# Performance work log

Measured on AMD Instinct MI355X. Metric: run time of the kernel, lower is better.

Reference implementation:

```python
import jax, jax.numpy as jnp
import numpy as np

N = 50000
E = 800000
IN_CH = 128
HID = 64
HEADS = 4
NEG_SLOPE_GAT = 0.2   # PyG GATConv default negative_slope
NEG_SLOPE_ACT = 0.01  # nn.LeakyReLU default
LN_EPS = 1e-5


def segment_softmax(logits, seg, num):
    # softmax over edges grouped by destination node (PyG softmax semantics)
    m = jax.ops.segment_max(logits, seg, num_segments=num)
    m = jnp.where(jnp.isfinite(m), m, 0.0)
    e = jnp.exp(logits - m[seg])
    s = jax.ops.segment_sum(e, seg, num_segments=num)
    return e / (s[seg] + 1e-16)


def gat_conv(x, edge_index, W, a_src, a_dst, b, heads, out_ch):
    n = x.shape[0]
    loop = jnp.arange(n)
    src = jnp.concatenate([edge_index[0], loop])  # message sources (x_j)
    dst = jnp.concatenate([edge_index[1], loop])  # aggregation targets (x_i)
    h = (x @ W).reshape(n, heads, out_ch)          # [N,H,C]
    alpha_src = (h * a_src).sum(-1)                # [N,H]
    alpha_dst = (h * a_dst).sum(-1)                # [N,H]
    alpha = alpha_src[src] + alpha_dst[dst]        # [E',H]
    alpha = jax.nn.leaky_relu(alpha, NEG_SLOPE_GAT)
    alpha = segment_softmax(alpha, dst, n)
    msg = h[src] * alpha[:, :, None]               # [E',H,C] gathered messages
    out = jax.ops.segment_sum(msg, dst, num_segments=n)  # [N,H,C]
    return out.reshape(n, heads * out_ch) + b


def layer_norm(x, gamma, beta):
    mu = x.mean(-1, keepdims=True)
    var = ((x - mu) ** 2).mean(-1, keepdims=True)
    return (x - mu) * jax.lax.rsqrt(var + LN_EPS) * gamma + beta


def setup_inputs() -> dict:
    key = jax.random.key(0)
    ks = jax.random.split(key, 12)
    d1 = HEADS * HID
    inp = {
        "x": jax.random.normal(ks[0], (N, IN_CH), dtype=jnp.float32),
        "edge_index": jax.random.randint(ks[1], (2, E), 0, N, dtype=jnp.int64),
        "W1": jax.random.normal(ks[2], (IN_CH, d1), dtype=jnp.float32) * 0.05,
        "a_src1": jax.random.normal(ks[3], (HEADS, HID), dtype=jnp.float32) * 0.1,
        "a_dst1": jax.random.normal(ks[4], (HEADS, HID), dtype=jnp.float32) * 0.1,
        "b1": jnp.zeros((d1,), dtype=jnp.float32),
        "gamma": jnp.ones((d1,), dtype=jnp.float32),
        "beta": jnp.zeros((d1,), dtype=jnp.float32),
        "W2": jax.random.normal(ks[5], (d1, HID), dtype=jnp.float32) * 0.05,
        "a_src2": jax.random.normal(ks[6], (1, HID), dtype=jnp.float32) * 0.1,
        "a_dst2": jax.random.normal(ks[7], (1, HID), dtype=jnp.float32) * 0.1,
        "b2": jnp.zeros((HID,), dtype=jnp.float32),
    }
    return inp


def reference(x, edge_index, W1, a_src1, a_dst1, b1, gamma, beta, W2, a_src2, a_dst2, b2):
    h = gat_conv(x, edge_index, W1, a_src1, a_dst1, b1, HEADS, HID)  # [N, H*HID]
    h = layer_norm(h, gamma, beta)
    h = jax.nn.leaky_relu(h, NEG_SLOPE_ACT)
    out = gat_conv(h, edge_index, W2, a_src2, a_dst2, b2, 1, HID)    # [N, HID]
    return out
```

## Files before the change

### kernel.cpp

```cpp
#include <hip/hip_runtime.h>
#include <hip/hip_bf16.h>

#define IN_CH 128
#define D1 256
#define HID 64
#define HEADS 4
#define CAP 48

typedef _Float16 h16;
typedef __attribute__((ext_vector_type(4))) _Float16 half4v;
typedef __attribute__((ext_vector_type(8))) _Float16 half8v;
typedef __attribute__((ext_vector_type(4))) float f32x4;

__device__ __forceinline__ float lrelu02(float v) { return v > 0.f ? v : 0.2f * v; }
__device__ __forceinline__ float lrelu001(float v) { return v > 0.f ? v : 0.01f * v; }
__device__ __forceinline__ unsigned short h2b(h16 h) {
    union { h16 h; unsigned short b; } c; c.h = h; return c.b;
}
__device__ __forceinline__ h16 b2h(unsigned short b) {
    union { unsigned short b; h16 h; } c; c.b = b; return c.h;
}

__global__ __launch_bounds__(256) void prep_kernel(const float* __restrict__ W1,
                                                   const float* __restrict__ W2,
                                                   const float* __restrict__ a_src1,
                                                   const float* __restrict__ a_dst1,
                                                   const float* __restrict__ a_src2,
                                                   const float* __restrict__ a_dst2,
                                                   h16* __restrict__ w1t,
                                                   h16* __restrict__ w2t) {
    const int b = blockIdx.x;
    const int t = threadIdx.x;
    if (b == 0) {
        for (int k = 0; k < IN_CH; ++k) w1t[t * IN_CH + k] = (h16)W1[k * D1 + t];
    } else if (b == 1) {
        if (t < HID)
            for (int k = 0; k < D1; ++k) w2t[t * D1 + k] = (h16)W2[k * HID + t];
        for (int i = t; i < 14 * D1; i += 256) w2t[66 * D1 + i] = (h16)0.f;
    } else if (b == 2) {
        for (int o = t; o < 1024; o += 256) {
            int v = o >> 7, k = o & 127;
            int h = v & 3;
            const float* avec = (v >> 2) ? (a_dst1 + h * HID) : (a_src1 + h * HID);
            const float* wrow = W1 + k * D1 + h * HID;
            float s = 0.f;
            for (int c = 0; c < HID; ++c) s += wrow[c] * avec[c];
            w1t[(256 + v) * IN_CH + k] = (h16)s;
            w1t[(264 + v) * IN_CH + k] = (h16)0.f;
        }
    } else {
        for (int o = t; o < 512; o += 256) {
            int v = o >> 8, k = o & 255;
            const float* avec = v ? a_dst2 : a_src2;
            const float* wrow = W2 + k * HID;
            float s = 0.f;
            for (int c = 0; c < HID; ++c) s += wrow[c] * avec[c];
            w2t[(64 + v) * D1 + k] = (h16)s;
        }
    }
}

__global__ __launch_bounds__(256) void gemm1_mfma(const float* __restrict__ x,
                                                  const h16* __restrict__ w1t,
                                                  h16* __restrict__ h1,
                                                  float* __restrict__ asad, int n) {
    const int wave = threadIdx.x >> 6, lane = threadIdx.x & 63;
    const int r = lane & 15, ksel = lane >> 4;
    const int rowBase = blockIdx.x * 64 + wave * 16;
    const int row_a = rowBase + r;
    half8v a[4];
    if (row_a < n) {
        const float* xrow = x + (size_t)row_a * IN_CH + ksel * 8;
        #pragma unroll
        for (int kk = 0; kk < 4; ++kk) {
            float4 u = *(const float4*)(xrow + kk * 32);
            float4 v = *(const float4*)(xrow + kk * 32 + 4);
            half8v av;
            av[0] = (h16)u.x; av[1] = (h16)u.y; av[2] = (h16)u.z; av[3] = (h16)u.w;
            av[4] = (h16)v.x; av[5] = (h16)v.y; av[6] = (h16)v.z; av[7] = (h16)v.w;
            a[kk] = av;
        }
    } else {
        #pragma unroll
        for (int kk = 0; kk < 4; ++kk) a[kk] = (half8v){};
    }
    f32x4 acc[17];
    #pragma unroll
    for (int ct = 0; ct < 17; ++ct) acc[ct] = (f32x4){0.f, 0.f, 0.f, 0.f};
    #pragma unroll
    for (int ct = 0; ct < 17; ++ct) {
        const h16* wrow = w1t + (size_t)(ct * 16 + r) * IN_CH + ksel * 8;
        #pragma unroll
        for (int kk = 0; kk < 4; ++kk) {
            half8v b = *(const half8v*)(wrow + kk * 32);
            acc[ct] = __builtin_amdgcn_mfma_f32_16x16x32_f16(a[kk], b, acc[ct], 0, 0, 0);
        }
    }
    #pragma unroll
    for (int i = 0; i < 4; ++i) {
        int row = rowBase + ksel * 4 + i;
        if (row < n) {
            #pragma unroll
            for (int ct = 0; ct < 16; ++ct)
                h1[(size_t)row * D1 + ct * 16 + r] = (h16)acc[ct][i];
            if (r < 8) asad[(size_t)row * 8 + r] = acc[16][i];
        }
    }
}

__global__ __launch_bounds__(256) void scatter_ewt_kernel(const int* __restrict__ ei,
                                                          int* __restrict__ cnt,
                                                          const float* __restrict__ asad,
                                                          int4* __restrict__ esd, int nE) {
    int e = blockIdx.x * 256 + threadIdx.x;
    if (e >= nE) return;
    int src = ei[e];
    int dst = ei[nE + e];
    int pos = atomicAdd(&cnt[dst], 1);
    if (pos >= CAP) return;
    float4 as = *(const float4*)&asad[(size_t)src * 8];
    float4 ad = *(const float4*)&asad[(size_t)dst * 8 + 4];
    unsigned short b0 = h2b((h16)expf(lrelu02(as.x + ad.x)));
    unsigned short b1 = h2b((h16)expf(lrelu02(as.y + ad.y)));
    unsigned short b2 = h2b((h16)expf(lrelu02(as.z + ad.z)));
    unsigned short b3 = h2b((h16)expf(lrelu02(as.w + ad.w)));
    int w01 = (int)b0 | ((int)b1 << 16);
    int w23 = (int)b2 | ((int)b3 << 16);
    esd[(size_t)dst * CAP + pos] = make_int4(src, w01, w23, 0);
}

__global__ __launch_bounds__(256) void gemm2_mfma(const h16* __restrict__ hm,
                                                  const h16* __restrict__ w2t,
                                                  h16* __restrict__ h2,
                                                  float* __restrict__ asad2, int n) {
    const int wave = threadIdx.x >> 6, lane = threadIdx.x & 63;
    const int r = lane & 15, ksel = lane >> 4;
    const int rowBase = blockIdx.x * 64 + wave * 16;
    const h16* xrow = hm + (size_t)(rowBase + r) * D1 + ksel * 8;
    half8v a[8];
    #pragma unroll
    for (int kk = 0; kk < 8; ++kk) a[kk] = *(const half8v*)(xrow + kk * 32);
    f32x4 acc[5];
    #pragma unroll
    for (int ct = 0; ct < 5; ++ct) acc[ct] = (f32x4){0.f, 0.f, 0.f, 0.f};
    #pragma unroll
    for (int ct = 0; ct < 5; ++ct) {
        const h16* wrow = w2t + (size_t)(ct * 16 + r) * D1 + ksel * 8;
        #pragma unroll
        for (int kk = 0; kk < 8; ++kk) {
            half8v b = *(const half8v*)(wrow + kk * 32);
            acc[ct] = __builtin_amdgcn_mfma_f32_16x16x32_f16(a[kk], b, acc[ct], 0, 0, 0);
        }
    }
    #pragma unroll
    for (int i = 0; i < 4; ++i) {
        int row = rowBase + ksel * 4 + i;
        if (row < n) {
            #pragma unroll
            for (int ct = 0; ct < 4; ++ct)
                h2[(size_t)row * HID + ct * 16 + r] = (h16)acc[ct][i];
            if (r < 2) asad2[(size_t)row * 2 + r] = acc[4][i];
        }
    }
}

__global__ __launch_bounds__(256) void gather1_kernel(const h16* __restrict__ h1,
                                                      const float* __restrict__ asad,
                                                      const int4* __restrict__ esd,
                                                      const int* __restrict__ cnt,
                                                      const float* __restrict__ b1,
                                                      const float* __restrict__ gamma,
                                                      const float* __restrict__ beta,
                                                      h16* __restrict__ hmid,
                                                      int n, int npad) {
    const int lane = threadIdx.x & 63;
    const int node = (blockIdx.x * 256 + threadIdx.x) >> 6;
    if (node >= npad) return;
    if (node >= n) {
        half4v z = {};
        *(half4v*)&hmid[(size_t)node * D1 + lane * 4] = z;
        return;
    }
    const int hh = lane >> 4;
    const int hsel = hh & 1;
    const unsigned* ep  = (const unsigned*)esd;
    const unsigned* epw = ep + 1 + (hh >> 1);
    const float wself = expf(lrelu02(asad[(size_t)node * 8 + hh] +
                                     asad[(size_t)node * 8 + 4 + hh]));
    half4v sv = *(const half4v*)&h1[(size_t)node * D1 + lane * 4];
    h16 wsh = (h16)wself;
    half4v acc = sv * (half4v){wsh, wsh, wsh, wsh};
    float den = wself;
    int d = cnt[node]; d = d < CAP ? d : CAP;
    const int beg = node * CAP;
    const int end = beg + ((d + 7) & ~7);
    int j = beg;
    for (; j + 8 <= end; j += 8) {
        int s0 = (int)ep[(size_t)(j + 0) * 4];
        int s1 = (int)ep[(size_t)(j + 1) * 4];
        int s2 = (int)ep[(size_t)(j + 2) * 4];
        int s3 = (int)ep[(size_t)(j + 3) * 4];
        int s4 = (int)ep[(size_t)(j + 4) * 4];
        int s5 = (int)ep[(size_t)(j + 5) * 4];
        int s6 = (int)ep[(size_t)(j + 6) * 4];
        int s7 = (int)ep[(size_t)(j + 7) * 4];
        unsigned u0 = epw[(size_t)(j + 0) * 4];
        unsigned u1 = epw[(size_t)(j + 1) * 4];
        unsigned u2 = epw[(size_t)(j + 2) * 4];
        unsigned u3 = epw[(size_t)(j + 3) * 4];
        unsigned u4 = epw[(size_t)(j + 4) * 4];
        unsigned u5 = epw[(size_t)(j + 5) * 4];
        unsigned u6 = epw[(size_t)(j + 6) * 4];
        unsigned u7 = epw[(size_t)(j + 7) * 4];
        half4v r0 = *(const half4v*)&h1[(size_t)s0 * D1 + lane * 4];
        half4v r1 = *(const half4v*)&h1[(size_t)s1 * D1 + lane * 4];
        half4v r2 = *(const half4v*)&h1[(size_t)s2 * D1 + lane * 4];
        half4v r3 = *(const half4v*)&h1[(size_t)s3 * D1 + lane * 4];
        half4v r4 = *(const half4v*)&h1[(size_t)s4 * D1 + lane * 4];
        half4v r5 = *(const half4v*)&h1[(size_t)s5 * D1 + lane * 4];
        half4v r6 = *(const half4v*)&h1[(size_t)s6 * D1 + lane * 4];
        half4v r7 = *(const half4v*)&h1[(size_t)s7 * D1 + lane * 4];
        h16 w0 = b2h((unsigned short)(hsel ? u0 >> 16 : u0 & 0xffff));
        h16 w1 = b2h((unsigned short)(hsel ? u1 >> 16 : u1 & 0xffff));
        h16 w2 = b2h((unsigned short)(hsel ? u2 >> 16 : u2 & 0xffff));
        h16 w3 = b2h((unsigned short)(hsel ? u3 >> 16 : u3 & 0xffff));
        h16 w4 = b2h((unsigned short)(hsel ? u4 >> 16 : u4 & 0xffff));
        h16 w5 = b2h((unsigned short)(hsel ? u5 >> 16 : u5 & 0xffff));
        h16 w6 = b2h((unsigned short)(hsel ? u6 >> 16 : u6 & 0xffff));
        h16 w7 = b2h((unsigned short)(hsel ? u7 >> 16 : u7 & 0xffff));
        acc += r0 * (half4v){w0, w0, w0, w0};
        acc += r1 * (half4v){w1, w1, w1, w1};
        acc += r2 * (half4v){w2, w2, w2, w2};
        acc += r3 * (half4v){w3, w3, w3, w3};
        acc += r4 * (half4v){w4, w4, w4, w4};
        acc += r5 * (half4v){w5, w5, w5, w5};
        acc += r6 * (half4v){w6, w6, w6, w6};
        acc += r7 * (half4v){w7, w7, w7, w7};
        den += (float)w0 + (float)w1 + (float)w2 + (float)w3
             + (float)w4 + (float)w5 + (float)w6 + (float)w7;
    }
    float4 accf = make_float4((float)acc[0], (float)acc[1], (float)acc[2], (float)acc[3]);
    float inv = 1.f / (den + 1e-16f);
    float4 bv = *(const float4*)&b1[lane * 4];
    float4 y;
    y.x = accf.x * inv + bv.x; y.y = accf.y * inv + bv.y;
    y.z = accf.z * inv + bv.z; y.w = accf.w * inv + bv.w;
    float s = y.x + y.y + y.z + y.w;
    #pragma unroll
    for (int off = 1; off < 64; off <<= 1) s += __shfl_xor(s, off, 64);
    float mu = s * (1.f / 256.f);
    float4 dx;
    dx.x = y.x - mu; dx.y = y.y - mu; dx.z = y.z - mu; dx.w = y.w - mu;
    float sq = dx.x * dx.x + dx.y * dx.y + dx.z * dx.z + dx.w * dx.w;
    #pragma unroll
    for (int off = 1; off < 64; off <<= 1) sq += __shfl_xor(sq, off, 64);
    float rs = rsqrtf(sq * (1.f / 256.f) + 1e-5f);
    float4 g = *(const float4*)&gamma[lane * 4];
    float4 be = *(const float4*)&beta[lane * 4];
    half4v o;
    o.x = (h16)lrelu001(dx.x * rs * g.x + be.x);
    o.y = (h16)lrelu001(dx.y * rs * g.y + be.y);
    o.z = (h16)lrelu001(dx.z * rs * g.z + be.z);
    o.w = (h16)lrelu001(dx.w * rs * g.w + be.w);
    *(half4v*)&hmid[(size_t)node * D1 + lane * 4] = o;
}

__global__ __launch_bounds__(256) void gather2_kernel(const h16* __restrict__ h2,
                                                      const float* __restrict__ asad2,
                                                      const int4* __restrict__ esd,
                                                      const int* __restrict__ cnt,
                                                      const float* __restrict__ b2,
                                                      float* __restrict__ out, int n) {
    const int lane = threadIdx.x & 63;
    const int node = (blockIdx.x * 256 + threadIdx.x) >> 6;
    if (node >= n) return;
    const int li = lane & 15, eh = lane >> 4;
    const int c0 = li * 4;
    const float ad_n = asad2[(size_t)node * 2 + 1];
    float acc[4] = {0.f, 0.f, 0.f, 0.f};
    float den = 0.f;
    if (eh == 0) {
        float w0 = expf(lrelu02(asad2[(size_t)node * 2] + ad_n));
        half4v sv = *(const half4v*)&h2[(size_t)node * HID + c0];
        #pragma unroll
        for (int i = 0; i < 4; ++i) acc[i] = (float)sv[i] * w0;
        den = w0;
    }
    int d = cnt[node]; d = d < CAP ? d : CAP;
    const int beg = node * CAP;
    const int end = beg + d;
    int j = beg;
    for (; j + 8 <= end; j += 8) {
        int s0 = esd[j + eh].x;
        int s1 = esd[j + 4 + eh].x;
        float a0 = asad2[(size_t)s0 * 2], a1 = asad2[(size_t)s1 * 2];
        half4v r0 = *(const half4v*)&h2[(size_t)s0 * HID + c0];
        half4v r1 = *(const half4v*)&h2[(size_t)s1 * HID + c0];
        float w0 = expf(lrelu02(a0 + ad_n));
        float w1 = expf(lrelu02(a1 + ad_n));
        #pragma unroll
        for (int i = 0; i < 4; ++i) {
            acc[i] = fmaf((float)r0[i], w0, acc[i]);
            acc[i] = fmaf((float)r1[i], w1, acc[i]);
        }
        den += w0 + w1;
    }
    for (; j < end; j += 4) {
        int e = j + eh;
        bool v = e < end;
        int s = v ? esd[e].x : 0;
        float w = v ? expf(lrelu02(asad2[(size_t)s * 2] + ad_n)) : 0.f;
        half4v r = *(const half4v*)&h2[(size_t)s * HID + c0];
        #pragma unroll
        for (int i = 0; i < 4; ++i) acc[i] = fmaf((float)r[i], w, acc[i]);
        den += w;
    }
    #pragma unroll
    for (int i = 0; i < 4; ++i) {
        acc[i] += __shfl_xor(acc[i], 32, 64);
        acc[i] += __shfl_xor(acc[i], 16, 64);
    }
    den += __shfl_xor(den, 32, 64);
    den += __shfl_xor(den, 16, 64);
    if (lane < 16) {
        float inv = 1.f / (den + 1e-16f);
        float4 bv = *(const float4*)&b2[c0];
        float4 o;
        o.x = acc[0] * inv + bv.x;
        o.y = acc[1] * inv + bv.y;
        o.z = acc[2] * inv + bv.z;
        o.w = acc[3] * inv + bv.w;
        *(float4*)&out[(size_t)node * HID + c0] = o;
    }
}

extern "C" void kernel_launch(void* const* d_in, const int* in_sizes, int n_in,
                              void* d_out, int out_size, void* d_ws, size_t ws_size,
                              hipStream_t stream) {
    const float* x      = (const float*)d_in[0];
    const int*   ei     = (const int*)d_in[1];
    const float* W1     = (const float*)d_in[2];
    const float* a_src1 = (const float*)d_in[3];
    const float* a_dst1 = (const float*)d_in[4];
    const float* b1     = (const float*)d_in[5];
    const float* gamma  = (const float*)d_in[6];
    const float* beta   = (const float*)d_in[7];
    const float* W2     = (const float*)d_in[8];
    const float* a_src2 = (const float*)d_in[9];
    const float* a_dst2 = (const float*)d_in[10];
    const float* b2     = (const float*)d_in[11];
    float* out = (float*)d_out;

    const int N = in_sizes[0] / IN_CH;
    const int E = in_sizes[1] / 2;
    const int NP = (N + 63) & ~63;

    float* ws = (float*)d_ws;
    size_t off = 0;
    h16*   h1   = (h16*)(ws + off); off += (size_t)128 * N;
    h16*   hmid = (h16*)(ws + off); off += (size_t)128 * NP;
    h16*   h2   = (h16*)(ws + off); off += (size_t)32 * N;
    float* asad = ws + off;         off += (size_t)8 * N;
    float* asad2= ws + off;         off += (size_t)2 * N;
    h16* w1t = (h16*)(ws + off); off += 17408;
    h16* w2t = (h16*)(ws + off); off += 10240;
    off = (off + 3) & ~(size_t)3;
    int* cnt = (int*)(ws + off); off += N;
    off = (off + 3) & ~(size_t)3;
    int4* esd = (int4*)(ws + off); off += (size_t)4 * ((size_t)N * CAP + 8);
    const size_t memsetBytes = (size_t)(ws + off) - (size_t)cnt;

    const int nodeBlocks  = (N + 3) / 4;
    const int nodeBlocksP = (NP + 3) / 4;
    const int nThreadBlocksE = (E + 255) / 256;

    hipMemsetAsync(cnt, 0, memsetBytes, stream);
    prep_kernel<<<4, 256, 0, stream>>>(W1, W2, a_src1, a_dst1, a_src2, a_dst2, w1t, w2t);
    gemm1_mfma<<<NP / 64, 256, 0, stream>>>(x, w1t, h1, asad, N);
    scatter_ewt_kernel<<<nThreadBlocksE, 256, 0, stream>>>(ei, cnt, asad, esd, E);
    gather1_kernel<<<nodeBlocksP, 256, 0, stream>>>(h1, asad, esd, cnt,
                                                    b1, gamma, beta, hmid, N, NP);
    gemm2_mfma<<<NP / 64, 256, 0, stream>>>(hmid, w2t, h2, asad2, N);
    gather2_kernel<<<nodeBlocks, 256, 0, stream>>>(h2, asad2, esd, cnt, b2, out, N);
}
```

Before: 226.9 us.

## Split attention-logit GEMM out and co-schedule main GEMM with edge scatter

The first GEMM is split in two. A small kernel computes only the per-node attention logits (asad), and the main 256-column projection is fused into the edge-scatter kernel as extra blocks. The scatter depends only on asad, so the compute-bound GEMM blocks and the atomic-heavy, memory-bound scatter blocks can run concurrently in one launch. In exchange, x is read twice, and one launch has to carry both the register-heavy MFMA path and the light scatter path, which may reduce occupancy for the scatter blocks.

```diff
diff --git a/kernel.cpp b/kernel.cpp
--- a/kernel.cpp
+++ b/kernel.cpp
@@ -60,10 +60,9 @@
     }
 }
 
-__global__ __launch_bounds__(256) void gemm1_mfma(const float* __restrict__ x,
-                                                  const h16* __restrict__ w1t,
-                                                  h16* __restrict__ h1,
-                                                  float* __restrict__ asad, int n) {
+__global__ __launch_bounds__(256) void asadg_kernel(const float* __restrict__ x,
+                                                    const h16* __restrict__ w1t,
+                                                    float* __restrict__ asad, int n) {
     const int wave = threadIdx.x >> 6, lane = threadIdx.x & 63;
     const int r = lane & 15, ksel = lane >> 4;
     const int rowBase = blockIdx.x * 64 + wave * 16;
@@ -84,11 +83,69 @@
         #pragma unroll
         for (int kk = 0; kk < 4; ++kk) a[kk] = (half8v){};
     }
-    f32x4 acc[17];
-    #pragma unroll
-    for (int ct = 0; ct < 17; ++ct) acc[ct] = (f32x4){0.f, 0.f, 0.f, 0.f};
-    #pragma unroll
-    for (int ct = 0; ct < 17; ++ct) {
+    f32x4 acc = (f32x4){0.f, 0.f, 0.f, 0.f};
+    const h16* wrow = w1t + (size_t)(256 + r) * IN_CH + ksel * 8;
+    #pragma unroll
+    for (int kk = 0; kk < 4; ++kk) {
+        half8v b = *(const half8v*)(wrow + kk * 32);
+        acc = __builtin_amdgcn_mfma_f32_16x16x32_f16(a[kk], b, acc, 0, 0, 0);
+    }
+    #pragma unroll
+    for (int i = 0; i < 4; ++i) {
+        int row = rowBase + ksel * 4 + i;
+        if (row < n && r < 8) asad[(size_t)row * 8 + r] = acc[i];
+    }
+}
+
+__global__ __launch_bounds__(256) void scatter_gemm1_kernel(
+        const int* __restrict__ ei, int* __restrict__ cnt,
+        const float* __restrict__ asad, int4* __restrict__ esd, int nE, int nbE,
+        const float* __restrict__ x, const h16* __restrict__ w1t,
+        h16* __restrict__ h1, int n) {
+    if (blockIdx.x < (unsigned)nbE) {
+        int e = blockIdx.x * 256 + threadIdx.x;
+        if (e >= nE) return;
+        int src = ei[e];
+        int dst = ei[nE + e];
+        int pos = atomicAdd(&cnt[dst], 1);
+        if (pos >= CAP) return;
+        float4 as = *(const float4*)&asad[(size_t)src * 8];
+        float4 ad = *(const float4*)&asad[(size_t)dst * 8 + 4];
+        unsigned short b0 = h2b((h16)expf(lrelu02(as.x + ad.x)));
+        unsigned short b1 = h2b((h16)expf(lrelu02(as.y + ad.y)));
+        unsigned short b2 = h2b((h16)expf(lrelu02(as.z + ad.z)));
+        unsigned short b3 = h2b((h16)expf(lrelu02(as.w + ad.w)));
+        int w01 = (int)b0 | ((int)b1 << 16);
+        int w23 = (int)b2 | ((int)b3 << 16);
+        esd[(size_t)dst * CAP + pos] = make_int4(src, w01, w23, 0);
+        return;
+    }
+    const int bid = blockIdx.x - nbE;
+    const int wave = threadIdx.x >> 6, lane = threadIdx.x & 63;
+    const int r = lane & 15, ksel = lane >> 4;
+    const int rowBase = bid * 64 + wave * 16;
+    const int row_a = rowBase + r;
+    half8v a[4];
+    if (row_a < n) {
+        const float* xrow = x + (size_t)row_a * IN_CH + ksel * 8;
+        #pragma unroll
+        for (int kk = 0; kk < 4; ++kk) {
+            float4 u = *(const float4*)(xrow + kk * 32);
+            float4 v = *(const float4*)(xrow + kk * 32 + 4);
+            half8v av;
+            av[0] = (h16)u.x; av[1] = (h16)u.y; av[2] = (h16)u.z; av[3] = (h16)u.w;
+            av[4] = (h16)v.x; av[5] = (h16)v.y; av[6] = (h16)v.z; av[7] = (h16)v.w;
+            a[kk] = av;
+        }
+    } else {
+        #pragma unroll
+        for (int kk = 0; kk < 4; ++kk) a[kk] = (half8v){};
+    }
+    f32x4 acc[16];
+    #pragma unroll
+    for (int ct = 0; ct < 16; ++ct) acc[ct] = (f32x4){0.f, 0.f, 0.f, 0.f};
+    #pragma unroll
+    for (int ct = 0; ct < 16; ++ct) {
         const h16* wrow = w1t + (size_t)(ct * 16 + r) * IN_CH + ksel * 8;
         #pragma unroll
         for (int kk = 0; kk < 4; ++kk) {
@@ -103,30 +160,8 @@
             #pragma unroll
             for (int ct = 0; ct < 16; ++ct)
                 h1[(size_t)row * D1 + ct * 16 + r] = (h16)acc[ct][i];
-            if (r < 8) asad[(size_t)row * 8 + r] = acc[16][i];
-        }
-    }
-}
-
-__global__ __launch_bounds__(256) void scatter_ewt_kernel(const int* __restrict__ ei,
-                                                          int* __restrict__ cnt,
-                                                          const float* __restrict__ asad,
-                                                          int4* __restrict__ esd, int nE) {
-    int e = blockIdx.x * 256 + threadIdx.x;
-    if (e >= nE) return;
-    int src = ei[e];
-    int dst = ei[nE + e];
-    int pos = atomicAdd(&cnt[dst], 1);
-    if (pos >= CAP) return;
-    float4 as = *(const float4*)&asad[(size_t)src * 8];
-    float4 ad = *(const float4*)&asad[(size_t)dst * 8 + 4];
-    unsigned short b0 = h2b((h16)expf(lrelu02(as.x + ad.x)));
-    unsigned short b1 = h2b((h16)expf(lrelu02(as.y + ad.y)));
-    unsigned short b2 = h2b((h16)expf(lrelu02(as.z + ad.z)));
-    unsigned short b3 = h2b((h16)expf(lrelu02(as.w + ad.w)));
-    int w01 = (int)b0 | ((int)b1 << 16);
-    int w23 = (int)b2 | ((int)b3 << 16);
-    esd[(size_t)dst * CAP + pos] = make_int4(src, w01, w23, 0);
+        }
+    }
 }
 
 __global__ __launch_bounds__(256) void gemm2_mfma(const h16* __restrict__ hm,
@@ -376,8 +411,9 @@
 
     hipMemsetAsync(cnt, 0, memsetBytes, stream);
     prep_kernel<<<4, 256, 0, stream>>>(W1, W2, a_src1, a_dst1, a_src2, a_dst2, w1t, w2t);
-    gemm1_mfma<<<NP / 64, 256, 0, stream>>>(x, w1t, h1, asad, N);
-    scatter_ewt_kernel<<<nThreadBlocksE, 256, 0, stream>>>(ei, cnt, asad, esd, E);
+    asadg_kernel<<<NP / 64, 256, 0, stream>>>(x, w1t, asad, N);
+    scatter_gemm1_kernel<<<nThreadBlocksE + NP / 64, 256, 0, stream>>>(
+        ei, cnt, asad, esd, E, nThreadBlocksE, x, w1t, h1, N);
     gather1_kernel<<<nodeBlocksP, 256, 0, stream>>>(h1, asad, esd, cnt,
                                                     b1, gamma, beta, hmid, N, NP);
     gemm2_mfma<<<NP / 64, 256, 0, stream>>>(hmid, w2t, h2, asad2, N);
```

Result: slower. 235.6 us (+3.8%).
